# Kernel tuning notes

Measured on AMD Instinct MI355X. Metric: run time of the kernel, lower is better.

The kernel has to match this reference:

```python
import jax, jax.numpy as jnp
import numpy as np

K, B, T, D = 4, 4096, 32, 128


def setup_inputs() -> dict:
    key = jax.random.key(0)
    k1, k2, k3 = jax.random.split(key, 3)
    semb = jax.random.normal(k1, (K, B, D), dtype=jnp.float32)
    slabels = jax.random.randint(k2, (K, B), 0, 2, dtype=jnp.int32)
    topk_ngh = jax.random.randint(k3, (K, B, T), 0, B, dtype=jnp.int32)
    return {"semb": semb, "slabels": slabels, "topk_ngh": topk_ngh}


def reference(semb, slabels, topk_ngh):
    """Dense, masked reformulation of DistanceLayer.forward (hardest=False).

    Original emits, per domain k and anchor i, one triplet for every pair
    (sn, dn) where sn/dn are topk neighbors of i with same/different binary
    label, carrying sim[i,sn] (pos_dist), sim[i,dn] (neg_dist) and the anchor/
    pos/neg embeddings. Here we return the same quantities densified over the
    fixed [K,B,T,T] pair grid with a validity mask (jit-compatible shapes).
    Anchor embeddings are semb itself; pos/neg embeddings are rows of
    nbr_embed selected by the same/diff sides of pair_mask.
    """
    gather = jax.vmap(lambda tbl, idx: tbl[idx])  # per-domain row gather
    nbr_embed = gather(semb, topk_ngh)            # [K,B,T,D]
    nbr_label = gather(slabels, topk_ngh)         # [K,B,T]
    # sim[i, ngh[i,t]] without materializing the full [B,B] sim matrix
    nsim = jnp.einsum('kbd,kbtd->kbt', semb, nbr_embed)  # [K,B,T]
    same = nbr_label == slabels[:, :, None]       # neighbor shares anchor label
    pair_mask = same[:, :, :, None] & (~same)[:, :, None, :]  # [K,B,T,T]
    pos_dist = jnp.where(pair_mask, nsim[:, :, :, None], 0.0)  # sim(i, sn)
    neg_dist = jnp.where(pair_mask, nsim[:, :, None, :], 0.0)  # sim(i, dn)
    return pos_dist, neg_dist, pair_mask, nbr_embed
```

## Files before the change

### kernel.cpp

```cpp
#include <hip/hip_runtime.h>
#include <hip/hip_bf16.h>

constexpr int K = 4;
constexpr int B = 4096;
constexpr int T = 32;
constexpr int D = 128;
constexpr int TT = T * T;
constexpr int TD = T * D;

typedef float f4 __attribute__((ext_vector_type(4)));

__global__ __launch_bounds__(256) void distance_layer_kernel(
    const float* __restrict__ semb,
    const int*   __restrict__ slabels,
    const int*   __restrict__ topk,
    float* __restrict__ pos,
    float* __restrict__ neg,
    float* __restrict__ maskf,
    float* __restrict__ nbr)
{
    const int kb  = blockIdx.x;
    const int k   = kb >> 12;
    const int tid = threadIdx.x;

    __shared__ f4    anchor4[D / 4];
    __shared__ int   idx_s[T];
    __shared__ float nsim_s[T];
    __shared__ int   same_s[T];

    const int my_label = slabels[kb];
    if (tid < T) {
        const int idx = topk[(size_t)kb * T + tid];
        idx_s[tid]  = idx;
        same_s[tid] = (slabels[k * B + idx] == my_label) ? 1 : 0;
    }
    if (tid < D / 4) {
        anchor4[tid] =
            reinterpret_cast<const f4*>(semb + (size_t)kb * D)[tid];
    }
    __syncthreads();

    const f4* semb4 = reinterpret_cast<const f4*>(semb + (size_t)k * B * D);
    f4*       nbr4  = reinterpret_cast<f4*>(nbr + (size_t)kb * TD);

    #pragma unroll
    for (int j = 0; j < 4; ++j) {
        const int c  = tid + 256 * j;
        const int t  = c >> 5;
        const int d4 = c & 31;
        const f4 a = anchor4[d4];
        const f4 s = semb4[(size_t)idx_s[t] * (D / 4) + d4];
        __builtin_nontemporal_store(s, nbr4 + c);
        float p = a.x * s.x + a.y * s.y + a.z * s.z + a.w * s.w;
        #pragma unroll
        for (int m = 16; m >= 1; m >>= 1)
            p += __shfl_xor(p, m, 64);
        if ((tid & 31) == 0) nsim_s[t] = p;
    }
    __syncthreads();

    f4* pos4  = reinterpret_cast<f4*>(pos   + (size_t)kb * TT);
    f4* neg4  = reinterpret_cast<f4*>(neg   + (size_t)kb * TT);
    f4* mask4 = reinterpret_cast<f4*>(maskf + (size_t)kb * TT);

    const int s_row = tid >> 3;
    const int d0    = (tid & 7) * 4;
    const int   ss = same_s[s_row];
    const float ps = nsim_s[s_row];

    f4 pv, nv, mv;
    {
        const int m0 = ss & (same_s[d0 + 0] ^ 1);
        const int m1 = ss & (same_s[d0 + 1] ^ 1);
        const int m2 = ss & (same_s[d0 + 2] ^ 1);
        const int m3 = ss & (same_s[d0 + 3] ^ 1);
        pv.x = m0 ? ps : 0.0f;  nv.x = m0 ? nsim_s[d0 + 0] : 0.0f;  mv.x = (float)m0;
        pv.y = m1 ? ps : 0.0f;  nv.y = m1 ? nsim_s[d0 + 1] : 0.0f;  mv.y = (float)m1;
        pv.z = m2 ? ps : 0.0f;  nv.z = m2 ? nsim_s[d0 + 2] : 0.0f;  mv.z = (float)m2;
        pv.w = m3 ? ps : 0.0f;  nv.w = m3 ? nsim_s[d0 + 3] : 0.0f;  mv.w = (float)m3;
    }
    __builtin_nontemporal_store(pv, pos4  + tid);
    __builtin_nontemporal_store(nv, neg4  + tid);
    __builtin_nontemporal_store(mv, mask4 + tid);
}

extern "C" void kernel_launch(void* const* d_in, const int* in_sizes, int n_in,
                              void* d_out, int out_size, void* d_ws, size_t ws_size,
                              hipStream_t stream) {
    const float* semb    = (const float*)d_in[0];
    const int*   slabels = (const int*)d_in[1];
    const int*   topk    = (const int*)d_in[2];

    float* out = (float*)d_out;
    const size_t KBTT = (size_t)K * B * T * T;
    float* pos   = out;
    float* neg   = out + KBTT;
    float* maskf = out + 2 * KBTT;
    float* nbr   = out + 3 * KBTT;

    distance_layer_kernel<<<dim3(K * B), dim3(256), 0, stream>>>(
        semb, slabels, topk, pos, neg, maskf, nbr);
}
```

Before: 463.9 us.

## Split into gather/nsim kernel and pair-output kernel via stash in mask buffer

Splits the single kernel into two launches. The first gathers neighbor rows with all four loads issued up front, computes the similarities, and writes them plus a ballot bitmask of same-label flags into the mask output region as scratch. The second kernel reads that stash and writes the pos, neg and mask tiles, overwriting the scratch in place. The aim is to separate the gather-heavy phase from the streaming-store phase and add memory-level parallelism, at the cost of an extra launch and a global round trip. There is also a sync inside k_pairs whose only role is to make every thread finish reading the stash before any thread overwrites it.

```diff
diff --git a/kernel.cpp b/kernel.cpp
--- a/kernel.cpp
+++ b/kernel.cpp
@@ -10,75 +10,110 @@
 
 typedef float f4 __attribute__((ext_vector_type(4)));
 
-__global__ __launch_bounds__(256) void distance_layer_kernel(
+__device__ __forceinline__ float dot4(f4 a, f4 b) {
+    return a.x * b.x + a.y * b.y + a.z * b.z + a.w * b.w;
+}
+
+__device__ __forceinline__ float hreduce32(float p) {
+    #pragma unroll
+    for (int m = 16; m >= 1; m >>= 1) p += __shfl_xor(p, m, 64);
+    return p;
+}
+
+__global__ __launch_bounds__(256) void k_gather_nsim(
     const float* __restrict__ semb,
     const int*   __restrict__ slabels,
     const int*   __restrict__ topk,
-    float* __restrict__ pos,
-    float* __restrict__ neg,
-    float* __restrict__ maskf,
-    float* __restrict__ nbr)
+    float* __restrict__ nbr,
+    float* __restrict__ stash)
 {
     const int kb  = blockIdx.x;
     const int k   = kb >> 12;
     const int tid = threadIdx.x;
 
-    __shared__ f4    anchor4[D / 4];
+    __shared__ f4    anchor4[T];
     __shared__ int   idx_s[T];
     __shared__ float nsim_s[T];
-    __shared__ int   same_s[T];
 
     const int my_label = slabels[kb];
+    int same = 0;
     if (tid < T) {
-        const int idx = topk[(size_t)kb * T + tid];
-        idx_s[tid]  = idx;
-        same_s[tid] = (slabels[k * B + idx] == my_label) ? 1 : 0;
-    }
-    if (tid < D / 4) {
+        const int idx = topk[kb * T + tid];
+        idx_s[tid] = idx;
+        same = (slabels[(k << 12) + idx] == my_label) ? 1 : 0;
         anchor4[tid] =
             reinterpret_cast<const f4*>(semb + (size_t)kb * D)[tid];
     }
+    const unsigned long long bal = __ballot(same);
     __syncthreads();
 
     const f4* semb4 = reinterpret_cast<const f4*>(semb + (size_t)k * B * D);
     f4*       nbr4  = reinterpret_cast<f4*>(nbr + (size_t)kb * TD);
 
-    #pragma unroll
-    for (int j = 0; j < 4; ++j) {
-        const int c  = tid + 256 * j;
-        const int t  = c >> 5;
-        const int d4 = c & 31;
-        const f4 a = anchor4[d4];
-        const f4 s = semb4[(size_t)idx_s[t] * (D / 4) + d4];
-        __builtin_nontemporal_store(s, nbr4 + c);
-        float p = a.x * s.x + a.y * s.y + a.z * s.z + a.w * s.w;
-        #pragma unroll
-        for (int m = 16; m >= 1; m >>= 1)
-            p += __shfl_xor(p, m, 64);
-        if ((tid & 31) == 0) nsim_s[t] = p;
+    const int w  = tid >> 5;
+    const int d4 = tid & 31;
+    const f4  a  = anchor4[d4];
+    const int i0 = idx_s[w], i1 = idx_s[8 + w], i2 = idx_s[16 + w], i3 = idx_s[24 + w];
+
+    const f4 s0 = semb4[(size_t)i0 * (D / 4) + d4];
+    const f4 s1 = semb4[(size_t)i1 * (D / 4) + d4];
+    const f4 s2 = semb4[(size_t)i2 * (D / 4) + d4];
+    const f4 s3 = semb4[(size_t)i3 * (D / 4) + d4];
+    __builtin_nontemporal_store(s0, nbr4 + ((0  + w) * (D / 4) + d4));
+    __builtin_nontemporal_store(s1, nbr4 + ((8  + w) * (D / 4) + d4));
+    __builtin_nontemporal_store(s2, nbr4 + ((16 + w) * (D / 4) + d4));
+    __builtin_nontemporal_store(s3, nbr4 + ((24 + w) * (D / 4) + d4));
+
+    const float p0 = hreduce32(dot4(a, s0));
+    const float p1 = hreduce32(dot4(a, s1));
+    const float p2 = hreduce32(dot4(a, s2));
+    const float p3 = hreduce32(dot4(a, s3));
+    if (d4 == 0) {
+        nsim_s[0  + w] = p0;
+        nsim_s[8  + w] = p1;
+        nsim_s[16 + w] = p2;
+        nsim_s[24 + w] = p3;
     }
     __syncthreads();
 
-    f4* pos4  = reinterpret_cast<f4*>(pos   + (size_t)kb * TT);
-    f4* neg4  = reinterpret_cast<f4*>(neg   + (size_t)kb * TT);
-    f4* mask4 = reinterpret_cast<f4*>(maskf + (size_t)kb * TT);
+    float* st = stash + (size_t)kb * TT;
+    if (tid < T) st[tid] = nsim_s[tid];
+    if (tid == 32)
+        reinterpret_cast<unsigned*>(st)[T] = (unsigned)bal;
+}
 
+__global__ __launch_bounds__(256) void k_pairs(
+    float* pos,
+    float* neg,
+    float* maskf)
+{
+    const int kb  = blockIdx.x;
+    const int tid = threadIdx.x;
+
+    float* st = maskf + (size_t)kb * TT;
+    const unsigned bits = reinterpret_cast<const unsigned*>(st)[T];
     const int s_row = tid >> 3;
-    const int d0    = (tid & 7) * 4;
-    const int   ss = same_s[s_row];
-    const float ps = nsim_s[s_row];
+    const int dq    = tid & 7;
+    const float ps  = st[s_row];
+    const f4    nd  = reinterpret_cast<const f4*>(st)[dq];
+    __syncthreads();
+
+    const int ss       = (bits >> s_row) & 1;
+    const unsigned ndb = ~(bits >> (dq * 4));
+    const int m0 = ss & (ndb & 1);
+    const int m1 = ss & ((ndb >> 1) & 1);
+    const int m2 = ss & ((ndb >> 2) & 1);
+    const int m3 = ss & ((ndb >> 3) & 1);
 
     f4 pv, nv, mv;
-    {
-        const int m0 = ss & (same_s[d0 + 0] ^ 1);
-        const int m1 = ss & (same_s[d0 + 1] ^ 1);
-        const int m2 = ss & (same_s[d0 + 2] ^ 1);
-        const int m3 = ss & (same_s[d0 + 3] ^ 1);
-        pv.x = m0 ? ps : 0.0f;  nv.x = m0 ? nsim_s[d0 + 0] : 0.0f;  mv.x = (float)m0;
-        pv.y = m1 ? ps : 0.0f;  nv.y = m1 ? nsim_s[d0 + 1] : 0.0f;  mv.y = (float)m1;
-        pv.z = m2 ? ps : 0.0f;  nv.z = m2 ? nsim_s[d0 + 2] : 0.0f;  mv.z = (float)m2;
-        pv.w = m3 ? ps : 0.0f;  nv.w = m3 ? nsim_s[d0 + 3] : 0.0f;  mv.w = (float)m3;
-    }
+    pv.x = m0 ? ps : 0.0f;  nv.x = m0 ? nd.x : 0.0f;  mv.x = (float)m0;
+    pv.y = m1 ? ps : 0.0f;  nv.y = m1 ? nd.y : 0.0f;  mv.y = (float)m1;
+    pv.z = m2 ? ps : 0.0f;  nv.z = m2 ? nd.z : 0.0f;  mv.z = (float)m2;
+    pv.w = m3 ? ps : 0.0f;  nv.w = m3 ? nd.w : 0.0f;  mv.w = (float)m3;
+
+    f4* pos4  = reinterpret_cast<f4*>(pos + (size_t)kb * TT);
+    f4* neg4  = reinterpret_cast<f4*>(neg + (size_t)kb * TT);
+    f4* mask4 = reinterpret_cast<f4*>(st);
     __builtin_nontemporal_store(pv, pos4  + tid);
     __builtin_nontemporal_store(nv, neg4  + tid);
     __builtin_nontemporal_store(mv, mask4 + tid);
@@ -98,6 +133,7 @@
     float* maskf = out + 2 * KBTT;
     float* nbr   = out + 3 * KBTT;
 
-    distance_layer_kernel<<<dim3(K * B), dim3(256), 0, stream>>>(
-        semb, slabels, topk, pos, neg, maskf, nbr);
+    k_gather_nsim<<<dim3(K * B), dim3(256), 0, stream>>>(
+        semb, slabels, topk, nbr, maskf);
+    k_pairs<<<dim3(K * B), dim3(256), 0, stream>>>(pos, neg, maskf);
 }
```

New measurement: 481.3 us. 1.04x slower.
